# Kernel tuning notes

Hardware: AMD Instinct MI355X
Metric: run time of the kernel (lower is better)

Reference implementation:

```python
import jax, jax.numpy as jnp
import numpy as np

DT = 0.1
B_SZ = 8192
T_HIST = 20
LEN_PRED = 30
FEAT = 32
N_LAYERS = 3
# state transition for constant-acceleration model (matches self.F in torch)
F_MAT = np.array([[1.0, DT, DT * DT / 2], [0.0, 1.0, DT], [0.0, 0.0, 1.0]], dtype=np.float32)


def setup_inputs() -> dict:
    key = jax.random.key(0)
    ks = jax.random.split(key, 16)
    # random-walk trajectories as history observations
    hist = jnp.cumsum(jax.random.normal(ks[0], (B_SZ, T_HIST, 2), jnp.float32) * 0.5, axis=1)
    k_lin = 1.0 / np.sqrt(FEAT)
    k_in = 1.0 / np.sqrt(24)

    def u(k, shape, scale):
        return jax.random.uniform(k, shape, jnp.float32, -scale, scale)

    return {
        "hist": hist,
        "max_accel_x": jnp.ones((1,), jnp.float32) * 10.0,
        "max_accel_y": jnp.ones((1,), jnp.float32) * 20.0,
        "velocity_std_x": jnp.ones((1,), jnp.float32) * 10.0,
        "acceleration_std_x": jnp.ones((1,), jnp.float32) * 10.0,
        "R_x_": jnp.array([0.0448], jnp.float32),
        "R_y_": jnp.array([0.001], jnp.float32),
        "G_x": jnp.array([0.0059, 0.2981, 0.0393], jnp.float32),
        "G_y": jnp.array([0.0059, 0.2981, 0.0393], jnp.float32) / 5.0,
        "Win_W": u(ks[1], (FEAT, 24), k_in),
        "Win_b": u(ks[2], (FEAT,), k_in),
        "enc_Wih": u(ks[3], (N_LAYERS, 4 * FEAT, FEAT), k_lin),
        "enc_Whh": u(ks[4], (N_LAYERS, 4 * FEAT, FEAT), k_lin),
        "enc_bih": u(ks[5], (N_LAYERS, 4 * FEAT), k_lin),
        "enc_bhh": u(ks[6], (N_LAYERS, 4 * FEAT), k_lin),
        "dec_Wih": u(ks[7], (N_LAYERS, 4 * FEAT, FEAT), k_lin),
        "dec_Whh": u(ks[8], (N_LAYERS, 4 * FEAT, FEAT), k_lin),
        "dec_bih": u(ks[9], (N_LAYERS, 4 * FEAT), k_lin),
        "dec_bhh": u(ks[10], (N_LAYERS, 4 * FEAT), k_lin),
        "Wout_W": u(ks[11], (4, FEAT), k_lin),
        "Wout_b": u(ks[12], (4,), k_lin),
        "len_pred": LEN_PRED,
    }


def reference(hist, max_accel_x, max_accel_y, velocity_std_x, acceleration_std_x,
              R_x_, R_y_, G_x, G_y, Win_W, Win_b,
              enc_Wih, enc_Whh, enc_bih, enc_bhh,
              dec_Wih, dec_Whh, dec_bih, dec_bhh,
              Wout_W, Wout_b, len_pred):
    B = hist.shape[0]
    F = jnp.asarray(F_MAT)
    R_x = R_x_[0] * R_x_[0]
    R_y = R_y_[0] * R_y_[0]
    Z_x = hist[:, :, 0]
    Z_y = hist[:, :, 1]

    def lstm(x, h, c, Wih, Whh, bih, bhh):
        g = x @ Wih.T + bih + h @ Whh.T + bhh
        i, f, gg, o = jnp.split(g, 4, axis=1)
        c = jax.nn.sigmoid(f) * c + jax.nn.sigmoid(i) * jnp.tanh(gg)
        h = jax.nn.sigmoid(o) * jnp.tanh(c)
        return h, c

    def stack(XP, h, c, Wih, Whh, bih, bhh):
        x = jnp.tanh(XP @ Win_W.T + Win_b)
        hs, cs = [], []
        for j in range(N_LAYERS):
            hj, cj = lstm(x, h[j], c[j], Wih[j], Whh[j], bih[j], bhh[j])
            hs.append(hj)
            cs.append(cj)
            x = cj  # torch code feeds the fresh CELL state to the next layer
        return jnp.stack(hs), jnp.stack(cs)

    def kpred(X, P, Q):
        return X @ F.T, jnp.einsum('ij,bjk,lk->bil', F, P, F) + Q

    def kupdate(X, P, z, R):
        y = z - X[:, 0]                      # innovation (H picks component 0)
        S = P[:, 0, 0] + R                   # innovation covariance (scalar)
        K = P[:, :, 0] / S[:, None]          # Kalman gain (B,3)
        return X + y[:, None] * K, P - K[:, :, None] * P[:, 0:1, :]

    def kinit(z0):
        # torch always calls _kalman_init with is_x=True (default), so both
        # axes use R_x / velocity_std_x / acceleration_std_x
        X = jnp.zeros((B, 3), hist.dtype).at[:, 0].set(z0)
        d = jnp.stack([R_x, velocity_std_x[0] ** 2, acceleration_std_x[0] ** 2])
        P = jnp.zeros((B, 3, 3), hist.dtype).at[:, jnp.arange(3), jnp.arange(3)].set(d)
        return X, P

    Qx_e = jnp.outer(G_x * max_accel_x[0], G_x * max_accel_x[0])
    Qy_e = jnp.outer(G_y * max_accel_y[0], G_y * max_accel_y[0])

    Xx, Px = kinit(Z_x[:, 0])
    Xy, Py = kinit(Z_y[:, 0])
    h = jnp.zeros((N_LAYERS, B, FEAT), hist.dtype)
    c = jnp.zeros_like(h)

    def enc_step(carry, zs):
        Xx, Px, Xy, Py, h, c = carry
        zx, zy = zs
        XP = jnp.concatenate([Xx, Xy, Px.reshape(B, 9), Py.reshape(B, 9)], 1)
        h, c = stack(XP, h, c, enc_Wih, enc_Whh, enc_bih, enc_bhh)
        Xx, Px = kpred(Xx, Px, Qx_e)
        Xy, Py = kpred(Xy, Py, Qy_e)
        Xx, Px = kupdate(Xx, Px, zx, R_x)
        Xy, Py = kupdate(Xy, Py, zy, R_y)
        return (Xx, Px, Xy, Py, h, c), None

    carry, _ = jax.lax.scan(enc_step, (Xx, Px, Xy, Py, h, c),
                            (Z_x[:, 1:].T, Z_y[:, 1:].T))

    oxx = jnp.outer(G_x, G_x)
    oyy = jnp.outer(G_y, G_y)

    def dec_step(carry, _):
        Xx, Px, Xy, Py, h, c = carry
        XP = jnp.concatenate([Xx, Xy, Px.reshape(B, 9), Py.reshape(B, 9)], 1)
        h, c = stack(XP, h, c, dec_Wih, dec_Whh, dec_bih, dec_bhh)
        pred = c[-1] @ Wout_W.T + Wout_b  # (B,4): [u_x, u_y, std_x, std_y]
        Xx = Xx.at[:, 2].set(DT * pred[:, 0])  # X[:,2] = B*u
        Xy = Xy.at[:, 2].set(DT * pred[:, 1])
        Qx = (pred[:, 2] ** 2)[:, None, None] * oxx
        Qy = (pred[:, 3] ** 2)[:, None, None] * oyy
        Xx, Px = kpred(Xx, Px, Qx)
        Xy, Py = kpred(Xy, Py, Qy)
        out = jnp.stack([Xx[:, 0], Xy[:, 0],
                         jnp.sqrt(Px[:, 0, 0]), jnp.sqrt(Py[:, 0, 0]),
                         jnp.zeros(B, hist.dtype)], axis=1)  # (B,5)
        return (Xx, Px, Xy, Py, h, c), out

    carry, ys = jax.lax.scan(dec_step, carry, None, length=len_pred)
    return jnp.transpose(ys, (1, 0, 2))  # (B, len_pred, 5)
```

## Files before the change

kernel.cpp:

```cpp
#include <hip/hip_runtime.h>
#include <math.h>

#define DT   0.1f
#define HDT  0.005f
#define T_HIST 20
#define LEN_PRED 30
#define NLOG2E   (-1.4426950408889634f)
#define TWOLOG2E ( 2.8853900817779268f)

typedef __attribute__((ext_vector_type(8))) short bfrag8;
typedef __attribute__((ext_vector_type(4))) float f32x4;

#define WS_FRAG  0u
#define WS_WIN   98304u
#define WS_WOUT  100352u
#define WS_BIASC 101376u
#define WS_WINC  102912u
#define WS_WOUTB 103040u

static __device__ __forceinline__ unsigned short f2bf(float x) {
    union { float f; unsigned int u; } v; v.f = x;
    unsigned int r = v.u + 0x7fffu + ((v.u >> 16) & 1u);
    return (unsigned short)(r >> 16);
}

static __device__ __forceinline__ unsigned int pack2bf(float lo, float hi) {
    unsigned int ul = __float_as_uint(lo) + 0x8000u;
    unsigned int uh = __float_as_uint(hi) + 0x8000u;
    return __builtin_amdgcn_perm(uh, ul, 0x07060302u);
}

static __device__ __forceinline__ float rcp1(float z) {
    return __builtin_amdgcn_rcpf(1.f + __builtin_amdgcn_exp2f(z));
}
static __device__ __forceinline__ float th_(float z) {
    return fmaf(-2.f, rcp1(z), 1.f);
}

__global__ void prep_kernel(const float* __restrict__ Win_W, const float* __restrict__ Win_b,
                            const float* __restrict__ eWih, const float* __restrict__ eWhh,
                            const float* __restrict__ ebih, const float* __restrict__ ebhh,
                            const float* __restrict__ dWih, const float* __restrict__ dWhh,
                            const float* __restrict__ dbih, const float* __restrict__ dbhh,
                            const float* __restrict__ Wout_W, const float* __restrict__ Wout_b,
                            char* __restrict__ ws)
{
    int i = blockIdx.x * blockDim.x + threadIdx.x;
    if (i < 49152) {
        int fi = i >> 9, w = i & 511;
        int lane = w >> 3, jj = w & 7;
        int c = fi & 1, j = (fi >> 1) & 7, pl = fi >> 4;
        int l = pl % 3, ph = pl / 3;
        int mm = lane & 15, qq = lane >> 4;
        int gate = mm & 3;
        int row = gate * 32 + 8 * (mm >> 2) + j;
        int k = qq * 8 + jj;
        float scale = (gate == 2) ? TWOLOG2E : NLOG2E;
        const float* W = c ? (ph ? dWhh : eWhh) : (ph ? dWih : eWih);
        ((unsigned short*)(ws + WS_FRAG))[i] = f2bf(W[l * 4096 + row * 32 + k] * scale);
    } else if (i < 50176) {
        int i2 = i - 49152;
        int T = i2 >> 9, w = i2 & 511;
        int lane = w >> 3, jj = w & 7;
        int mm = lane & 15, qq = lane >> 4;
        int feat = 8 * (mm >> 2) + 4 * T + (mm & 3);
        int k = qq * 8 + jj;
        float v = (k < 24) ? Win_W[feat * 24 + k] * TWOLOG2E : 0.f;
        ((unsigned short*)(ws + WS_WIN))[i2] = f2bf(v);
    } else if (i < 50688) {
        int i3 = i - 50176;
        int lane = i3 >> 3, jj = i3 & 7;
        int mm = lane & 15, qq = lane >> 4;
        float v = (mm < 4) ? Wout_W[mm * 32 + qq * 8 + jj] : 0.f;
        ((unsigned short*)(ws + WS_WOUT))[i3] = f2bf(v);
    } else if (i < 51072) {
        int b = i - 50688;
        int r = b & 3, qq = (b >> 2) & 3, j = (b >> 4) & 7, pl = b >> 7;
        int l = pl % 3, ph = pl / 3;
        int row = r * 32 + 8 * qq + j;
        float scale = (r == 2) ? TWOLOG2E : NLOG2E;
        const float* bi = ph ? dbih : ebih;
        const float* bh = ph ? dbhh : ebhh;
        ((float*)(ws + WS_BIASC))[b] = (bi[l * 128 + row] + bh[l * 128 + row]) * scale;
    } else if (i < 51104) {
        int b = i - 51072;
        int r = b & 3, qq = (b >> 2) & 3, T = b >> 4;
        ((float*)(ws + WS_WINC))[b] = Win_b[8 * qq + 4 * T + r] * TWOLOG2E;
    } else if (i < 51108) {
        ((float*)(ws + WS_WOUTB))[i - 51104] = Wout_b[i - 51104];
    }
}

__launch_bounds__(64)
__global__ void kalman_lstm_kernel(const float* __restrict__ hist,
                                   const float* __restrict__ max_ax, const float* __restrict__ max_ay,
                                   const float* __restrict__ vstd, const float* __restrict__ astd,
                                   const float* __restrict__ Rx_, const float* __restrict__ Ry_,
                                   const float* __restrict__ Gx, const float* __restrict__ Gy,
                                   const char* __restrict__ ws, float* __restrict__ out)
{
    __shared__ unsigned short xp[16][40];

    const int lane = threadIdx.x;
    const int q = lane >> 4, m = lane & 15, ch = q & 1;
    const bool act = (m < 8);
    const int b_elem = blockIdx.x * 8 + (m & 7);

    for (int i = lane; i < 640; i += 64) (&xp[0][0])[i] = 0;
    __builtin_amdgcn_wave_barrier();

    bfrag8 fragA[3][8][2];
    f32x4  biasC[3][8];
    const bfrag8* fragp = (const bfrag8*)(ws + WS_FRAG);
    const f32x4*  biasp = (const f32x4*)(ws + WS_BIASC);
    auto load_phase = [&](int ph) {
#pragma unroll
        for (int l = 0; l < 3; ++l)
#pragma unroll
            for (int j = 0; j < 8; ++j) {
#pragma unroll
                for (int c = 0; c < 2; ++c)
                    fragA[l][j][c] = fragp[(((ph * 3 + l) * 8 + j) * 2 + c) * 64 + lane];
                biasC[l][j] = biasp[((ph * 3 + l) * 8 + j) * 4 + q];
            }
    };
    load_phase(0);

    bfrag8 winF0 = ((const bfrag8*)(ws + WS_WIN))[lane];
    bfrag8 winF1 = ((const bfrag8*)(ws + WS_WIN))[64 + lane];
    f32x4  winC0 = ((const f32x4*)(ws + WS_WINC))[q];
    f32x4  winC1 = ((const f32x4*)(ws + WS_WINC))[4 + q];
    bfrag8 woutF = ((const bfrag8*)(ws + WS_WOUT))[lane];
    const float* wbp = (const float*)(ws + WS_WOUTB);
    const float wb0 = wbp[0], wb1 = wbp[1], wb2 = wbp[2], wb3 = wbp[3];

    const float rx = Rx_[0] * Rx_[0], ry = Ry_[0] * Ry_[0];
    const float Rch = ch ? ry : rx;
    float g0, g1, g2, s;
    if (ch == 0) { g0 = Gx[0]; g1 = Gx[1]; g2 = Gx[2]; s = max_ax[0]; }
    else         { g0 = Gy[0]; g1 = Gy[1]; g2 = Gy[2]; s = max_ay[0]; }
    const float ge0 = g0 * s, ge1 = g1 * s, ge2 = g2 * s;
    float X0 = (q < 2 && act) ? hist[b_elem * 40 + ch] : 0.f;
    float X1 = 0.f, X2 = 0.f;
    float P00 = Rch, P01 = 0.f, P02 = 0.f;
    float P11 = vstd[0] * vstd[0], P12 = 0.f, P22 = astd[0] * astd[0];

    union { unsigned int u[4]; bfrag8 v; } zf; zf.u[0] = zf.u[1] = zf.u[2] = zf.u[3] = 0;
    bfrag8 hfrag[3] = { zf.v, zf.v, zf.v };
    bfrag8 xfrag = zf.v;
    float cst[3][4];
#pragma unroll
    for (int l = 0; l < 3; ++l)
#pragma unroll
        for (int k = 0; k < 4; ++k) cst[l][k] = 0.f;

    auto kpred = [&](float Q00, float Q01, float Q02, float Q11, float Q12, float Q22) {
        X0 = X0 + DT * X1 + HDT * X2;
        X1 = X1 + DT * X2;
        float M00 = P00 + DT * P01 + HDT * P02;
        float M01 = P01 + DT * P11 + HDT * P12;
        float M02 = P02 + DT * P12 + HDT * P22;
        float M11 = P11 + DT * P12;
        float M12 = P12 + DT * P22;
        float M22 = P22;
        P00 = M00 + DT * M01 + HDT * M02 + Q00;
        P01 = M01 + DT * M02 + Q01;
        P02 = M02 + Q02;
        P11 = M11 + DT * M12 + Q11;
        P12 = M12 + Q12;
        P22 = M22 + Q22;
    };
    auto kupdate = [&](float z) {
        float y = z - X0;
        float Sinv = 1.0f / (P00 + Rch);
        float K0 = P00 * Sinv, K1 = P01 * Sinv, K2 = P02 * Sinv;
        X0 += y * K0; X1 += y * K1; X2 += y * K2;
        float p00 = P00, p01 = P01, p02 = P02;
        P00 = p00 - K0 * p00;
        P01 = p01 - K0 * p01;
        P02 = p02 - K0 * p02;
        P11 = P11 - K1 * p01;
        P12 = P12 - K1 * p02;
        P22 = P22 - K2 * p02;
    };

    auto stack = [&]() {
        if (q < 2 && act) {
            unsigned short* row = &xp[m][0];
            int o = ch * 3;
            row[o + 0] = f2bf(X0); row[o + 1] = f2bf(X1); row[o + 2] = f2bf(X2);
            int pb = 6 + ch * 9;
            row[pb + 0] = f2bf(P00); row[pb + 1] = f2bf(P01); row[pb + 2] = f2bf(P02);
            row[pb + 3] = f2bf(P01); row[pb + 4] = f2bf(P11); row[pb + 5] = f2bf(P12);
            row[pb + 6] = f2bf(P02); row[pb + 7] = f2bf(P12); row[pb + 8] = f2bf(P22);
        }
        __builtin_amdgcn_wave_barrier();
        bfrag8 bxp = *(const bfrag8*)&xp[m][q * 8];
        __builtin_amdgcn_wave_barrier();
        f32x4 t0 = __builtin_amdgcn_mfma_f32_16x16x32_bf16(winF0, bxp, winC0, 0, 0, 0);
        f32x4 t1 = __builtin_amdgcn_mfma_f32_16x16x32_bf16(winF1, bxp, winC1, 0, 0, 0);
        union { unsigned int u[4]; bfrag8 v; } xu;
        xu.u[0] = pack2bf(th_(t0[0]), th_(t0[1]));
        xu.u[1] = pack2bf(th_(t0[2]), th_(t0[3]));
        xu.u[2] = pack2bf(th_(t1[0]), th_(t1[1]));
        xu.u[3] = pack2bf(th_(t1[2]), th_(t1[3]));
        xfrag = xu.v;
#pragma unroll
        for (int l = 0; l < 3; ++l) {
            f32x4 acc[8];
#pragma unroll
            for (int j = 0; j < 8; ++j) {
                f32x4 hh = __builtin_amdgcn_mfma_f32_16x16x32_bf16(fragA[l][j][1], hfrag[l], biasC[l][j], 0, 0, 0);
                acc[j]   = __builtin_amdgcn_mfma_f32_16x16x32_bf16(fragA[l][j][0], xfrag, hh, 0, 0, 0);
            }
            float cn[4], hn[4];
#pragma unroll
            for (int k = 0; k < 4; ++k) {
                float s0 = __shfl_xor(acc[k + 4][0], 8);
                float s1 = __shfl_xor(acc[k + 4][1], 8);
                float s2 = __shfl_xor(acc[k + 4][2], 8);
                float s3 = __shfl_xor(acc[k + 4][3], 8);
                float gi = act ? acc[k][0] : s0;
                float gf = act ? acc[k][1] : s1;
                float gg = act ? acc[k][2] : s2;
                float go = act ? acc[k][3] : s3;
                float iv = rcp1(gi);
                float fv = rcp1(gf);
                float gv = th_(gg);
                float ov = rcp1(go);
                float cv = fmaf(fv, cst[l][k], iv * gv);
                cst[l][k] = cv;
                cn[k] = cv;
                hn[k] = ov * th_(cv * TWOLOG2E);
            }
            union { unsigned int u[4]; bfrag8 v; } xv, hv;
            xv.u[0] = pack2bf(cn[0], cn[1]); xv.u[1] = pack2bf(cn[2], cn[3]);
            hv.u[0] = pack2bf(hn[0], hn[1]); hv.u[1] = pack2bf(hn[2], hn[3]);
            xv.u[2] = __shfl_xor(xv.u[0], 8); xv.u[3] = __shfl_xor(xv.u[1], 8);
            hv.u[2] = __shfl_xor(hv.u[0], 8); hv.u[3] = __shfl_xor(hv.u[1], 8);
            xfrag = xv.v;
            hfrag[l] = hv.v;
        }
    };

    const f32x4 zero4 = {0.f, 0.f, 0.f, 0.f};

    float znext = (q < 2 && act) ? hist[b_elem * 40 + 2 + ch] : 0.f;
#pragma unroll 1
    for (int t = 0; t < T_HIST - 1; ++t) {
        stack();
        float z = znext;
        if (t < 18) znext = (q < 2 && act) ? hist[b_elem * 40 + (t + 2) * 2 + ch] : 0.f;
        kpred(ge0 * ge0, ge0 * ge1, ge0 * ge2, ge1 * ge1, ge1 * ge2, ge2 * ge2);
        kupdate(z);
    }

    load_phase(1);

#pragma unroll 1
    for (int t = 0; t < LEN_PRED; ++t) {
        stack();
        f32x4 ap = __builtin_amdgcn_mfma_f32_16x16x32_bf16(woutF, xfrag, zero4, 0, 0, 0);
        float s0 = __shfl(ap[0] + wb0, m);
        float s1 = __shfl(ap[1] + wb1, m);
        float s2 = __shfl(ap[2] + wb2, m);
        float s3 = __shfl(ap[3] + wb3, m);
        float pe = ch ? s1 : s0;
        float qe = ch ? s3 : s2;
        X2 = DT * pe;
        float qs = qe * qe;
        kpred(qs * g0 * g0, qs * g0 * g1, qs * g0 * g2, qs * g1 * g1, qs * g1 * g2, qs * g2 * g2);
        if (q < 2 && act) {
            float* o = out + (size_t)b_elem * (LEN_PRED * 5) + t * 5;
            if (ch == 0) { o[0] = X0; o[2] = sqrtf(P00); }
            else         { o[1] = X0; o[3] = sqrtf(P00); o[4] = 0.f; }
        }
    }
}

extern "C" void kernel_launch(void* const* d_in, const int* in_sizes, int n_in,
                              void* d_out, int out_size, void* d_ws, size_t ws_size,
                              hipStream_t stream)
{
    const float* hist  = (const float*)d_in[0];
    const float* maxax = (const float*)d_in[1];
    const float* maxay = (const float*)d_in[2];
    const float* vstd  = (const float*)d_in[3];
    const float* astd  = (const float*)d_in[4];
    const float* Rx    = (const float*)d_in[5];
    const float* Ry    = (const float*)d_in[6];
    const float* Gx    = (const float*)d_in[7];
    const float* Gy    = (const float*)d_in[8];
    const float* WinW  = (const float*)d_in[9];
    const float* Winb  = (const float*)d_in[10];
    const float* eWih  = (const float*)d_in[11];
    const float* eWhh  = (const float*)d_in[12];
    const float* ebih  = (const float*)d_in[13];
    const float* ebhh  = (const float*)d_in[14];
    const float* dWih  = (const float*)d_in[15];
    const float* dWhh  = (const float*)d_in[16];
    const float* dbih  = (const float*)d_in[17];
    const float* dbhh  = (const float*)d_in[18];
    const float* WoutW = (const float*)d_in[19];
    const float* Woutb = (const float*)d_in[20];
    char* ws = (char*)d_ws;
    float* out = (float*)d_out;

    prep_kernel<<<200, 256, 0, stream>>>(WinW, Winb, eWih, eWhh, ebih, ebhh,
                                         dWih, dWhh, dbih, dbhh, WoutW, Woutb, ws);
    kalman_lstm_kernel<<<1024, 64, 0, stream>>>(hist, maxax, maxay, vstd, astd,
                                                Rx, Ry, Gx, Gy, ws, out);
}
```

Baseline: 212.1 us.

## Replace shuffles with DPP row rotations and merge LSTM gate reciprocals

Replaces __shfl_xor lane exchanges, which go through LDS bpermute, with DPP row_ror:8 moves that stay in registers. The LSTM cell update is rewritten so the sigmoid and tanh gates share fewer reciprocals, with exp2 inputs clamped to avoid overflow. The input-projection tanh is split so each half-wave evaluates only half the values and then exchanges packed results. The aim is to shorten the per-step latency chain of the recurrent loop, at the cost of slightly different rounding and reliance on clamping for stability.

```diff
diff --git a/kernel.cpp b/kernel.cpp
--- a/kernel.cpp
+++ b/kernel.cpp
@@ -7,6 +7,7 @@
 #define LEN_PRED 30
 #define NLOG2E   (-1.4426950408889634f)
 #define TWOLOG2E ( 2.8853900817779268f)
+#define ECLAMP   40.0f
 
 typedef __attribute__((ext_vector_type(8))) short bfrag8;
 typedef __attribute__((ext_vector_type(4))) float f32x4;
@@ -30,6 +31,16 @@
     return __builtin_amdgcn_perm(uh, ul, 0x07060302u);
 }
 
+static __device__ __forceinline__ unsigned int dpp8i(unsigned int x) {
+    return (unsigned int)__builtin_amdgcn_update_dpp(0, (int)x, 0x128, 0xf, 0xf, true);
+}
+static __device__ __forceinline__ float dpp8f(float x) {
+    return __int_as_float(__builtin_amdgcn_update_dpp(0, __float_as_int(x), 0x128, 0xf, 0xf, true));
+}
+
+static __device__ __forceinline__ float exp2c(float z) {
+    return __builtin_amdgcn_exp2f(fminf(z, ECLAMP));
+}
 static __device__ __forceinline__ float rcp1(float z) {
     return __builtin_amdgcn_rcpf(1.f + __builtin_amdgcn_exp2f(z));
 }
@@ -199,12 +210,22 @@
         __builtin_amdgcn_wave_barrier();
         f32x4 t0 = __builtin_amdgcn_mfma_f32_16x16x32_bf16(winF0, bxp, winC0, 0, 0, 0);
         f32x4 t1 = __builtin_amdgcn_mfma_f32_16x16x32_bf16(winF1, bxp, winC1, 0, 0, 0);
-        union { unsigned int u[4]; bfrag8 v; } xu;
-        xu.u[0] = pack2bf(th_(t0[0]), th_(t0[1]));
-        xu.u[1] = pack2bf(th_(t0[2]), th_(t0[3]));
-        xu.u[2] = pack2bf(th_(t1[0]), th_(t1[1]));
-        xu.u[3] = pack2bf(th_(t1[2]), th_(t1[3]));
-        xfrag = xu.v;
+        float wv[4];
+#pragma unroll
+        for (int r = 0; r < 4; ++r) {
+            float sp = dpp8f(t1[r]);
+            wv[r] = th_(act ? t0[r] : sp);
+        }
+        {
+            unsigned int pk0 = pack2bf(wv[0], wv[1]), pk1 = pack2bf(wv[2], wv[3]);
+            unsigned int r0 = dpp8i(pk0), r1 = dpp8i(pk1);
+            union { unsigned int u[4]; bfrag8 v; } xu;
+            xu.u[0] = act ? pk0 : r0;
+            xu.u[1] = act ? pk1 : r1;
+            xu.u[2] = act ? r0 : pk0;
+            xu.u[3] = act ? r1 : pk1;
+            xfrag = xu.v;
+        }
 #pragma unroll
         for (int l = 0; l < 3; ++l) {
             f32x4 acc[8];
@@ -216,28 +237,32 @@
             float cn[4], hn[4];
 #pragma unroll
             for (int k = 0; k < 4; ++k) {
-                float s0 = __shfl_xor(acc[k + 4][0], 8);
-                float s1 = __shfl_xor(acc[k + 4][1], 8);
-                float s2 = __shfl_xor(acc[k + 4][2], 8);
-                float s3 = __shfl_xor(acc[k + 4][3], 8);
+                float s0 = dpp8f(acc[k + 4][0]);
+                float s1 = dpp8f(acc[k + 4][1]);
+                float s2 = dpp8f(acc[k + 4][2]);
+                float s3 = dpp8f(acc[k + 4][3]);
                 float gi = act ? acc[k][0] : s0;
                 float gf = act ? acc[k][1] : s1;
                 float gg = act ? acc[k][2] : s2;
                 float go = act ? acc[k][3] : s3;
-                float iv = rcp1(gi);
-                float fv = rcp1(gf);
-                float gv = th_(gg);
-                float ov = rcp1(go);
-                float cv = fmaf(fv, cst[l][k], iv * gv);
+                float I = exp2c(gi), F = exp2c(gf), G = exp2c(gg), O = exp2c(go);
+                float a  = 1.f + I, b = 1.f + F;
+                float gp = G + 1.f, gm = G - 1.f;
+                float D1  = a * gp;
+                float num = fmaf(cst[l][k], D1, gm * b);
+                float den = b * D1;
+                float cv  = num * __builtin_amdgcn_rcpf(den);
                 cst[l][k] = cv;
                 cn[k] = cv;
-                hn[k] = ov * th_(cv * TWOLOG2E);
+                float Ec = exp2c(cv * TWOLOG2E);
+                float em = Ec - 1.f, ep = Ec + 1.f, o1 = 1.f + O;
+                hn[k] = em * __builtin_amdgcn_rcpf(o1 * ep);
             }
             union { unsigned int u[4]; bfrag8 v; } xv, hv;
             xv.u[0] = pack2bf(cn[0], cn[1]); xv.u[1] = pack2bf(cn[2], cn[3]);
             hv.u[0] = pack2bf(hn[0], hn[1]); hv.u[1] = pack2bf(hn[2], hn[3]);
-            xv.u[2] = __shfl_xor(xv.u[0], 8); xv.u[3] = __shfl_xor(xv.u[1], 8);
-            hv.u[2] = __shfl_xor(hv.u[0], 8); hv.u[3] = __shfl_xor(hv.u[1], 8);
+            xv.u[2] = dpp8i(xv.u[0]); xv.u[3] = dpp8i(xv.u[1]);
+            hv.u[2] = dpp8i(hv.u[0]); hv.u[3] = dpp8i(hv.u[1]);
             xfrag = xv.v;
             hfrag[l] = hv.v;
         }
```

New measurement: 201.0 us. 1.06x faster.
